# Kernel optimization log

Measured on AMD Instinct MI355X. Metric: run time of the kernel, lower is better.

The kernel has to match this reference:

```python
import jax, jax.numpy as jnp
import numpy as np

B, T, C, H = 2, 2048, 1024, 16
D = C // H  # head_dim = 64

def setup_inputs() -> dict:
    key = jax.random.key(0)
    ks = jax.random.split(key, 5)
    x = jax.random.normal(ks[0], (B, T, C), dtype=jnp.float32)
    Wqkv = jax.random.normal(ks[1], (C, 3 * C), dtype=jnp.float32) * 0.02
    bqkv = jnp.zeros((3 * C,), dtype=jnp.float32)
    Wout = jax.random.normal(ks[2], (C, C), dtype=jnp.float32) * 0.02
    bout = jnp.zeros((C,), dtype=jnp.float32)
    return {"x": x, "Wqkv": Wqkv, "bqkv": bqkv, "Wout": Wout, "bout": bout}

def reference(x, Wqkv, bqkv, Wout, bout):
    Bb, Tt, Cc = x.shape
    qkv = x @ Wqkv + bqkv                       # [B,T,3C]
    qkv = qkv.reshape(Bb, Tt, 3, H, D)
    qkv = jnp.transpose(qkv, (2, 0, 3, 1, 4))   # [3,B,H,T,D]
    q, k, v = qkv[0], qkv[1], qkv[2]
    scale = 1.0 / np.sqrt(D).astype(np.float32)
    scores = jnp.einsum('bhqd,bhkd->bhqk', q, k) * scale  # [B,H,T,T]
    causal = jnp.tril(jnp.ones((Tt, Tt), dtype=bool))
    scores = jnp.where(causal[None, None, :, :], scores, jnp.float32(-jnp.inf))
    attn = jax.nn.softmax(scores, axis=-1)
    out = jnp.einsum('bhqk,bhkd->bhqd', attn, v)          # [B,H,T,D]
    out = jnp.transpose(out, (0, 2, 1, 3)).reshape(Bb, Tt, Cc)
    return out @ Wout + bout
```

## Files before the change

### kernel.cpp

```cpp
#include <hip/hip_runtime.h>

#define Bc 2
#define Tc 2048
#define Cc 1024
#define Hc 16
#define Dc 64
#define Mtot (Bc*Tc)
#define Kdim Cc
#define N1 (3*Cc)
#define N2 Cc

typedef __attribute__((ext_vector_type(8))) short short8;
typedef __attribute__((ext_vector_type(4))) float float4v;
typedef __attribute__((ext_vector_type(2))) unsigned int uint2v;
typedef __attribute__((ext_vector_type(4))) unsigned int uint4v;

#define HAVE_PLSWAP (__has_builtin(__builtin_amdgcn_permlane32_swap) && __has_builtin(__builtin_amdgcn_permlane16_swap))

__device__ __forceinline__ unsigned short f2bf(float f) {
  unsigned int u = __builtin_bit_cast(unsigned int, f);
  u += 0x7FFFu + ((u >> 16) & 1u);
  return (unsigned short)(u >> 16);
}

__device__ __forceinline__ unsigned int pk_bf16(float a, float b) {
#if __has_builtin(__builtin_amdgcn_cvt_pk_bf16_f32)
  typedef __attribute__((ext_vector_type(2))) __bf16 bf16x2;
  bf16x2 v = __builtin_amdgcn_cvt_pk_bf16_f32(a, b);
  return __builtin_bit_cast(unsigned int, v);
#else
  return (unsigned int)f2bf(a) | ((unsigned int)f2bf(b) << 16);
#endif
}

__device__ __forceinline__ float fast_exp2(float x) {
#if __has_builtin(__builtin_amdgcn_exp2f)
  return __builtin_amdgcn_exp2f(x);
#else
  return exp2f(x);
#endif
}

__device__ __forceinline__ void gl2lds16(const unsigned short* g, unsigned short* l) {
  __builtin_amdgcn_global_load_lds((const __attribute__((address_space(1))) void*)g,
                                   (__attribute__((address_space(3))) void*)l, 16, 0, 0);
}

#if HAVE_PLSWAP
__device__ __forceinline__ short8 pv_frag(unsigned int a, unsigned int b,
                                          unsigned int c, unsigned int d) {
  uint2v r0 = __builtin_amdgcn_permlane32_swap(a, c, false, false);
  uint2v r1 = __builtin_amdgcn_permlane16_swap(r0[0], r0[1], false, false);
  uint2v r2 = __builtin_amdgcn_permlane32_swap(b, d, false, false);
  uint2v r3 = __builtin_amdgcn_permlane16_swap(r2[0], r2[1], false, false);
  uint4v w = {r1[0], r3[0], r1[1], r3[1]};
  return __builtin_bit_cast(short8, w);
}
#endif

__global__ __launch_bounds__(256) void k_prep(const float* __restrict__ wqkv,
                                              const float* __restrict__ wout,
                                              const float* __restrict__ x,
                                              unsigned short* __restrict__ wqkvT,
                                              unsigned short* __restrict__ woutT,
                                              unsigned short* __restrict__ xb) {
  const int bx = blockIdx.x;
  if (bx >= 128) {
    int idx = ((bx - 128) * 32 + blockIdx.y) * 256 + threadIdx.x;
    float4 v = ((const float4*)x)[idx];
    uint2 o;
    o.x = pk_bf16(v.x, v.y);
    o.y = pk_bf16(v.z, v.w);
    ((uint2*)xb)[idx] = o;
    return;
  }
  __shared__ float tile[32][33];
  const float* w;  unsigned short* wT;  int N, n0;
  if (bx < 96) { w = wqkv; wT = wqkvT; N = N1; n0 = bx * 32; }
  else         { w = wout; wT = woutT; N = N2; n0 = (bx - 96) * 32; }
  const int k0 = blockIdx.y * 32;
  int tx = threadIdx.x & 31, ty = threadIdx.x >> 5;
  for (int i = 0; i < 4; ++i)
    tile[ty + 8*i][tx] = w[(size_t)(k0 + ty + 8*i) * N + n0 + tx];
  __syncthreads();
  for (int i = 0; i < 4; ++i)
    wT[(size_t)(n0 + ty + 8*i) * Kdim + k0 + tx] = f2bf(tile[tx][ty + 8*i]);
}

__global__ __launch_bounds__(256) void k_gemm_qkv(const unsigned short* __restrict__ A,
                                                  const unsigned short* __restrict__ BT,
                                                  const float* __restrict__ bias,
                                                  unsigned short* __restrict__ qkv) {
  __shared__ alignas(16) unsigned short smem[16384];
  const int m0 = blockIdx.y * 128, n0 = blockIdx.x * 128;
  const int tid = threadIdx.x;
  const int w = tid >> 6, lane = tid & 63;
  const int ln = lane & 15, qd = lane >> 4;
  const int wm = w >> 1, wn = w & 1;
  const int c0 = tid, c1 = tid + 256;
  const int row0 = c0 >> 2, ko0 = (c0 & 3) * 8;
  const int row1 = c1 >> 2, ko1 = (c1 & 3) * 8;
  const float4v zero4 = {0.f, 0.f, 0.f, 0.f};
  float4v acc[4][4];
  for (int i = 0; i < 4; ++i) for (int j = 0; j < 4; ++j) acc[i][j] = zero4;

  gl2lds16(A  + (size_t)(m0 + row0) * Kdim + ko0, smem + c0 * 8);
  gl2lds16(A  + (size_t)(m0 + row1) * Kdim + ko1, smem + c1 * 8);
  gl2lds16(BT + (size_t)(n0 + row0) * Kdim + ko0, smem + 4096 + c0 * 8);
  gl2lds16(BT + (size_t)(n0 + row1) * Kdim + ko1, smem + 4096 + c1 * 8);

  int cur = 0;
  for (int kk = 0; kk < Kdim; kk += 32) {
    __syncthreads();
    if (kk + 32 < Kdim) {
      unsigned short* nb = smem + (cur ^ 1) * 8192;
      gl2lds16(A  + (size_t)(m0 + row0) * Kdim + kk + 32 + ko0, nb + c0 * 8);
      gl2lds16(A  + (size_t)(m0 + row1) * Kdim + kk + 32 + ko1, nb + c1 * 8);
      gl2lds16(BT + (size_t)(n0 + row0) * Kdim + kk + 32 + ko0, nb + 4096 + c0 * 8);
      gl2lds16(BT + (size_t)(n0 + row1) * Kdim + kk + 32 + ko1, nb + 4096 + c1 * 8);
    }
    const unsigned short* As = smem + cur * 8192;
    const unsigned short* Bs = As + 4096;
    short8 af[4], bf[4];
    for (int i = 0; i < 4; ++i)
      af[i] = *(const short8*)(As + (wm*64 + i*16 + ln) * 32 + qd*8);
    for (int j = 0; j < 4; ++j)
      bf[j] = *(const short8*)(Bs + (wn*64 + j*16 + ln) * 32 + qd*8);
    for (int i = 0; i < 4; ++i)
      for (int j = 0; j < 4; ++j)
        acc[i][j] = __builtin_amdgcn_mfma_f32_16x16x32_bf16(af[i], bf[j], acc[i][j], 0, 0, 0);
    cur ^= 1;
  }
  const int s = n0 >> 10;
  if (s < 2) {
    const float scale = (s == 0) ? 0.125f : 1.0f;
    for (int i = 0; i < 4; ++i) {
      int mbase = m0 + wm*64 + i*16 + qd*4;
      for (int j = 0; j < 4; ++j) {
        int ncol = n0 + wn*64 + j*16 + ln;
        float bv = bias[ncol];
        int rem = ncol & 1023;
        int h = rem >> 6, d = rem & 63;
        for (int r = 0; r < 4; ++r) {
          int m = mbase + r;
          int b = m >> 11, t = m & 2047;
          float val = (acc[i][j][r] + bv) * scale;
          qkv[((((size_t)s*Bc + b)*Hc + h)*Tc + t)*Dc + d] = f2bf(val);
        }
      }
    }
  } else {
    unsigned short* vbase = qkv + (size_t)2*Bc*Hc*Tc*Dc;
    const int b = m0 >> 11, t0 = m0 & 2047;
    const int h0 = (n0 & 1023) >> 6;
    for (int p = 0; p < 2; ++p) {
      __syncthreads();
      if (wn == p) {
        for (int i = 0; i < 4; ++i) {
          int tl = wm*64 + i*16 + qd*4;
          for (int j = 0; j < 4; ++j) {
            int dl = j*16 + ln;
            float bv = bias[n0 + p*64 + dl];
            uint2 pk;
            pk.x = pk_bf16(acc[i][j][0] + bv, acc[i][j][1] + bv);
            pk.y = pk_bf16(acc[i][j][2] + bv, acc[i][j][3] + bv);
            *(uint2*)(smem + dl*136 + tl) = pk;
          }
        }
      }
      __syncthreads();
      for (int ii = 0; ii < 4; ++ii) {
        int idx = tid + 256*ii;
        int row = idx >> 4, c16 = idx & 15;
        int4 v = *(const int4*)(smem + row*136 + c16*8);
        *(int4*)(vbase + (((size_t)b*Hc + h0 + p)*Dc + row)*Tc + t0 + c16*8) = v;
      }
    }
  }
}

__global__ __launch_bounds__(256) void k_gemm_out(const unsigned short* __restrict__ A,
                                                  const unsigned short* __restrict__ BT,
                                                  const float* __restrict__ bias,
                                                  float* __restrict__ out) {
  __shared__ alignas(16) unsigned short smem[16384];
  const int m0 = blockIdx.y * 128, n0 = blockIdx.x * 128;
  const int tid = threadIdx.x;
  const int w = tid >> 6, lane = tid & 63;
  const int ln = lane & 15, qd = lane >> 4;
  const int wm = w >> 1, wn = w & 1;
  const int c0 = tid, c1 = tid + 256;
  const int row0 = c0 >> 2, ko0 = (c0 & 3) * 8;
  const int row1 = c1 >> 2, ko1 = (c1 & 3) * 8;
  const float4v zero4 = {0.f, 0.f, 0.f, 0.f};
  float4v acc[4][4];
  for (int i = 0; i < 4; ++i) for (int j = 0; j < 4; ++j) acc[i][j] = zero4;

  gl2lds16(A  + (size_t)(m0 + row0) * Kdim + ko0, smem + c0 * 8);
  gl2lds16(A  + (size_t)(m0 + row1) * Kdim + ko1, smem + c1 * 8);
  gl2lds16(BT + (size_t)(n0 + row0) * Kdim + ko0, smem + 4096 + c0 * 8);
  gl2lds16(BT + (size_t)(n0 + row1) * Kdim + ko1, smem + 4096 + c1 * 8);

  int cur = 0;
  for (int kk = 0; kk < Kdim; kk += 32) {
    __syncthreads();
    if (kk + 32 < Kdim) {
      unsigned short* nb = smem + (cur ^ 1) * 8192;
      gl2lds16(A  + (size_t)(m0 + row0) * Kdim + kk + 32 + ko0, nb + c0 * 8);
      gl2lds16(A  + (size_t)(m0 + row1) * Kdim + kk + 32 + ko1, nb + c1 * 8);
      gl2lds16(BT + (size_t)(n0 + row0) * Kdim + kk + 32 + ko0, nb + 4096 + c0 * 8);
      gl2lds16(BT + (size_t)(n0 + row1) * Kdim + kk + 32 + ko1, nb + 4096 + c1 * 8);
    }
    const unsigned short* As = smem + cur * 8192;
    const unsigned short* Bs = As + 4096;
    short8 af[4], bf[4];
    for (int i = 0; i < 4; ++i)
      af[i] = *(const short8*)(As + (wm*64 + i*16 + ln) * 32 + qd*8);
    for (int j = 0; j < 4; ++j)
      bf[j] = *(const short8*)(Bs + (wn*64 + j*16 + ln) * 32 + qd*8);
    for (int i = 0; i < 4; ++i)
      for (int j = 0; j < 4; ++j)
        acc[i][j] = __builtin_amdgcn_mfma_f32_16x16x32_bf16(af[i], bf[j], acc[i][j], 0, 0, 0);
    cur ^= 1;
  }
  for (int i = 0; i < 4; ++i) {
    int mbase = m0 + wm*64 + i*16 + qd*4;
    for (int j = 0; j < 4; ++j) {
      int ncol = n0 + wn*64 + j*16 + ln;
      float bv = bias[ncol];
      for (int r = 0; r < 4; ++r)
        out[(size_t)(mbase + r) * N2 + ncol] = acc[i][j][r] + bv;
    }
  }
}

__device__ __forceinline__ void attn_substep(
    const short8* kf, const short8* va,
    unsigned short* __restrict__ pw,
    const short8 qa0, const short8 qa1,
    float4v* o, float& l_part,
    int k0, int myq, bool mask, int ln, int qd)
{
  const float L2E = 1.44269504f;
  const float SH = 23.0831098f;
  const float4v zero4 = {0.f, 0.f, 0.f, 0.f};
  float4v s[4];
  for (int ki = 0; ki < 4; ++ki) {
    float4v z = zero4;
    z = __builtin_amdgcn_mfma_f32_16x16x32_bf16(kf[2*ki],     qa0, z, 0, 0, 0);
    s[ki] = __builtin_amdgcn_mfma_f32_16x16x32_bf16(kf[2*ki+1], qa1, z, 0, 0, 0);
  }
  if (mask) {
    for (int ki = 0; ki < 4; ++ki) {
      int key = k0 + ki*16 + qd*4;
      for (int r = 0; r < 4; ++r)
        if (key + r > myq) s[ki][r] = -1e30f;
    }
  }
  float st = 0.f;
  unsigned int pkw[4][2];
  for (int ki = 0; ki < 4; ++ki) {
    float p0 = fast_exp2(fmaf(s[ki][0], L2E, -SH));
    float p1 = fast_exp2(fmaf(s[ki][1], L2E, -SH));
    float p2 = fast_exp2(fmaf(s[ki][2], L2E, -SH));
    float p3 = fast_exp2(fmaf(s[ki][3], L2E, -SH));
    st += (p0 + p1) + (p2 + p3);
    pkw[ki][0] = pk_bf16(p0, p1);
    pkw[ki][1] = pk_bf16(p2, p3);
  }
  l_part += st;
#if HAVE_PLSWAP
  short8 pb0 = pv_frag(pkw[0][0], pkw[0][1], pkw[1][0], pkw[1][1]);
  short8 pb1 = pv_frag(pkw[2][0], pkw[2][1], pkw[3][0], pkw[3][1]);
#else
  for (int ki = 0; ki < 4; ++ki) {
    uint2 pk2; pk2.x = pkw[ki][0]; pk2.y = pkw[ki][1];
    *(uint2*)(pw + ln*72 + ki*16 + qd*4) = pk2;
  }
  short8 pb0 = *(const short8*)(pw + ln*72 + qd*8);
  short8 pb1 = *(const short8*)(pw + ln*72 + 32 + qd*8);
#endif
  for (int dt = 0; dt < 4; ++dt) {
    o[dt] = __builtin_amdgcn_mfma_f32_16x16x32_bf16(va[2*dt],   pb0, o[dt], 0, 0, 0);
    o[dt] = __builtin_amdgcn_mfma_f32_16x16x32_bf16(va[2*dt+1], pb1, o[dt], 0, 0, 0);
  }
}

__global__ __launch_bounds__(256) void k_attn(const unsigned short* __restrict__ qb,
                                              const unsigned short* __restrict__ kb,
                                              const unsigned short* __restrict__ vT,
                                              unsigned short* __restrict__ ob) {
  __shared__ alignas(16) unsigned short Ks[2][64*72];
  __shared__ alignas(16) unsigned short Vt[2][64*72];
#if !HAVE_PLSWAP
  __shared__ alignas(16) unsigned short Ps[4][16*72];
#endif
  const int bh = blockIdx.x;
  const int qt = 31 - blockIdx.y;
  const int tid = threadIdx.x;
  const int w = tid >> 6, lane = tid & 63;
  const int ln = lane & 15, qd = lane >> 4;
  const size_t base = (size_t)bh * Tc * Dc;
  const int b = bh >> 4, h = bh & 15;
  const int srow = tid >> 3, scol = (tid & 7) * 8;
  const float4v zero4 = {0.f, 0.f, 0.f, 0.f};
#if HAVE_PLSWAP
  unsigned short* pw = nullptr;
#else
  unsigned short* pw = Ps[w];
#endif

  const int myq = qt*64 + w*16 + ln;
  const unsigned short* qr = qb + base + (size_t)myq * Dc;
  short8 qa0 = *(const short8*)(qr + qd*8);
  short8 qa1 = *(const short8*)(qr + 32 + qd*8);
  float4v o[4];
  for (int dt = 0; dt < 4; ++dt) o[dt] = zero4;
  float l = 0.f;

  {
    int4 k0v = *(const int4*)(kb + base + (size_t)srow * Dc + scol);
    int4 k1v = *(const int4*)(kb + base + (size_t)(srow + 32) * Dc + scol);
    int4 v0v = *(const int4*)(vT + base + (size_t)srow * Tc + scol);
    int4 v1v = *(const int4*)(vT + base + (size_t)(srow + 32) * Tc + scol);
    *(int4*)(Ks[0] + srow*72 + scol)      = k0v;
    *(int4*)(Ks[0] + (srow+32)*72 + scol) = k1v;
    *(int4*)(Vt[0] + srow*72 + scol)      = v0v;
    *(int4*)(Vt[0] + (srow+32)*72 + scol) = v1v;
  }
  __syncthreads();

  for (int kt = 0; kt <= qt; ++kt) {
    const int cur = kt & 1;
    int4 rk0, rk1, rv0, rv1;
    if (kt < qt) {
      const int k0n = (kt + 1) * 64;
      rk0 = *(const int4*)(kb + base + (size_t)(k0n + srow) * Dc + scol);
      rk1 = *(const int4*)(kb + base + (size_t)(k0n + srow + 32) * Dc + scol);
      rv0 = *(const int4*)(vT + base + (size_t)srow * Tc + k0n + scol);
      rv1 = *(const int4*)(vT + base + (size_t)(srow + 32) * Tc + k0n + scol);
    }
    short8 kf[8], va[8];
    for (int ki = 0; ki < 4; ++ki) {
      const unsigned short* kr = Ks[cur] + (ki*16 + ln)*72;
      kf[2*ki]   = *(const short8*)(kr + qd*8);
      kf[2*ki+1] = *(const short8*)(kr + 32 + qd*8);
    }
    for (int dt = 0; dt < 4; ++dt) {
      const unsigned short* vr = Vt[cur] + (dt*16 + ln)*72;
      va[2*dt]   = *(const short8*)(vr + qd*8);
      va[2*dt+1] = *(const short8*)(vr + 32 + qd*8);
    }
    __builtin_amdgcn_s_setprio(1);
    attn_substep(kf, va, pw, qa0, qa1, o, l, kt*64, myq, kt == qt, ln, qd);
    __builtin_amdgcn_s_setprio(0);
    if (kt < qt) {
      const int nxt = cur ^ 1;
      *(int4*)(Ks[nxt] + srow*72 + scol)      = rk0;
      *(int4*)(Ks[nxt] + (srow+32)*72 + scol) = rk1;
      *(int4*)(Vt[nxt] + srow*72 + scol)      = rv0;
      *(int4*)(Vt[nxt] + (srow+32)*72 + scol) = rv1;
      __syncthreads();
    }
  }
  l += __shfl_xor(l, 16); l += __shfl_xor(l, 32);
  float inv = 1.0f / l;
  for (int dt = 0; dt < 4; ++dt) {
    uint2 ov;
    ov.x = pk_bf16(o[dt][0] * inv, o[dt][1] * inv);
    ov.y = pk_bf16(o[dt][2] * inv, o[dt][3] * inv);
    *(uint2*)(ob + (size_t)(b*Tc + myq)*Cc + h*Dc + dt*16 + qd*4) = ov;
  }
}

extern "C" void kernel_launch(void* const* d_in, const int* in_sizes, int n_in,
                              void* d_out, int out_size, void* d_ws, size_t ws_size,
                              hipStream_t stream) {
  const float* x    = (const float*)d_in[0];
  const float* Wqkv = (const float*)d_in[1];
  const float* bqkv = (const float*)d_in[2];
  const float* Wout = (const float*)d_in[3];
  const float* bout = (const float*)d_in[4];
  float* out = (float*)d_out;

  char* ws = (char*)d_ws;
  unsigned short* xb    = (unsigned short*)ws;
  unsigned short* wqkvT = (unsigned short*)(ws + 8388608);
  unsigned short* woutT = (unsigned short*)(ws + 14680064);
  unsigned short* qkvb  = (unsigned short*)(ws + 16777216);

  k_prep<<<dim3(256, 32), 256, 0, stream>>>(Wqkv, Wout, x, wqkvT, woutT, xb);
  k_gemm_qkv<<<dim3(N1/128, Mtot/128), 256, 0, stream>>>(xb, wqkvT, bqkv, qkvb);
  k_attn<<<dim3(32, 32), 256, 0, stream>>>(qkvb, qkvb + (size_t)Bc*Hc*Tc*Dc,
                                           qkvb + (size_t)2*Bc*Hc*Tc*Dc, xb);
  k_gemm_out<<<dim3(N2/128, Mtot/128), 256, 0, stream>>>(xb, woutT, bout, out);
}
```

Measured before the change: 177.0 us.

## Split attention key tile across warps and swizzle GEMM block order

The attention kernel now assigns each warp two 16-row query fragments and half of the 64-key tile, rather than one query fragment over all keys. K and V fragments loaded from LDS are reused across the two query fragments, and the two key-half partial outputs are combined through shared memory at the end. Both GEMM kernels also remap block indices with a swizzle so that consecutively scheduled blocks share tiles in cache. The costs are more accumulator registers per warp and an extra LDS reduction with two barriers.

```diff
diff --git a/kernel.cpp b/kernel.cpp
--- a/kernel.cpp
+++ b/kernel.cpp
@@ -92,7 +92,9 @@
                                                   const float* __restrict__ bias,
                                                   unsigned short* __restrict__ qkv) {
   __shared__ alignas(16) unsigned short smem[16384];
-  const int m0 = blockIdx.y * 128, n0 = blockIdx.x * 128;
+  const int lin = blockIdx.y * 24 + blockIdx.x;
+  const int swz = (lin & 7) * 96 + (lin >> 3);
+  const int m0 = (swz / 24) * 128, n0 = (swz % 24) * 128;
   const int tid = threadIdx.x;
   const int w = tid >> 6, lane = tid & 63;
   const int ln = lane & 15, qd = lane >> 4;
@@ -184,7 +186,9 @@
                                                   const float* __restrict__ bias,
                                                   float* __restrict__ out) {
   __shared__ alignas(16) unsigned short smem[16384];
-  const int m0 = blockIdx.y * 128, n0 = blockIdx.x * 128;
+  const int lin = blockIdx.y * 8 + blockIdx.x;
+  const int swz = (lin & 7) * 32 + (lin >> 3);
+  const int m0 = (swz >> 3) * 128, n0 = (swz & 7) * 128;
   const int tid = threadIdx.x;
   const int w = tid >> 6, lane = tid & 63;
   const int ln = lane & 15, qd = lane >> 4;
@@ -234,32 +238,32 @@
   }
 }
 
-__device__ __forceinline__ void attn_substep(
+__device__ __forceinline__ void attn_half(
     const short8* kf, const short8* va,
     unsigned short* __restrict__ pw,
     const short8 qa0, const short8 qa1,
     float4v* o, float& l_part,
-    int k0, int myq, bool mask, int ln, int qd)
+    int keybase, int myq, bool mask, int ln, int qd)
 {
   const float L2E = 1.44269504f;
   const float SH = 23.0831098f;
   const float4v zero4 = {0.f, 0.f, 0.f, 0.f};
-  float4v s[4];
-  for (int ki = 0; ki < 4; ++ki) {
+  float4v s[2];
+  for (int ki = 0; ki < 2; ++ki) {
     float4v z = zero4;
     z = __builtin_amdgcn_mfma_f32_16x16x32_bf16(kf[2*ki],     qa0, z, 0, 0, 0);
     s[ki] = __builtin_amdgcn_mfma_f32_16x16x32_bf16(kf[2*ki+1], qa1, z, 0, 0, 0);
   }
   if (mask) {
-    for (int ki = 0; ki < 4; ++ki) {
-      int key = k0 + ki*16 + qd*4;
+    for (int ki = 0; ki < 2; ++ki) {
+      int key = keybase + ki*16 + qd*4;
       for (int r = 0; r < 4; ++r)
         if (key + r > myq) s[ki][r] = -1e30f;
     }
   }
   float st = 0.f;
-  unsigned int pkw[4][2];
-  for (int ki = 0; ki < 4; ++ki) {
+  unsigned int pkw[2][2];
+  for (int ki = 0; ki < 2; ++ki) {
     float p0 = fast_exp2(fmaf(s[ki][0], L2E, -SH));
     float p1 = fast_exp2(fmaf(s[ki][1], L2E, -SH));
     float p2 = fast_exp2(fmaf(s[ki][2], L2E, -SH));
@@ -270,20 +274,16 @@
   }
   l_part += st;
 #if HAVE_PLSWAP
-  short8 pb0 = pv_frag(pkw[0][0], pkw[0][1], pkw[1][0], pkw[1][1]);
-  short8 pb1 = pv_frag(pkw[2][0], pkw[2][1], pkw[3][0], pkw[3][1]);
+  short8 pb = pv_frag(pkw[0][0], pkw[0][1], pkw[1][0], pkw[1][1]);
 #else
-  for (int ki = 0; ki < 4; ++ki) {
+  for (int ki = 0; ki < 2; ++ki) {
     uint2 pk2; pk2.x = pkw[ki][0]; pk2.y = pkw[ki][1];
     *(uint2*)(pw + ln*72 + ki*16 + qd*4) = pk2;
   }
-  short8 pb0 = *(const short8*)(pw + ln*72 + qd*8);
-  short8 pb1 = *(const short8*)(pw + ln*72 + 32 + qd*8);
-#endif
-  for (int dt = 0; dt < 4; ++dt) {
-    o[dt] = __builtin_amdgcn_mfma_f32_16x16x32_bf16(va[2*dt],   pb0, o[dt], 0, 0, 0);
-    o[dt] = __builtin_amdgcn_mfma_f32_16x16x32_bf16(va[2*dt+1], pb1, o[dt], 0, 0, 0);
-  }
+  short8 pb = *(const short8*)(pw + ln*72 + qd*8);
+#endif
+  for (int dt = 0; dt < 4; ++dt)
+    o[dt] = __builtin_amdgcn_mfma_f32_16x16x32_bf16(va[dt], pb, o[dt], 0, 0, 0);
 }
 
 __global__ __launch_bounds__(256) void k_attn(const unsigned short* __restrict__ qb,
@@ -300,6 +300,7 @@
   const int tid = threadIdx.x;
   const int w = tid >> 6, lane = tid & 63;
   const int ln = lane & 15, qd = lane >> 4;
+  const int kw = w >> 1, qw = w & 1;
   const size_t base = (size_t)bh * Tc * Dc;
   const int b = bh >> 4, h = bh & 15;
   const int srow = tid >> 3, scol = (tid & 7) * 8;
@@ -310,13 +311,16 @@
   unsigned short* pw = Ps[w];
 #endif
 
-  const int myq = qt*64 + w*16 + ln;
-  const unsigned short* qr = qb + base + (size_t)myq * Dc;
-  short8 qa0 = *(const short8*)(qr + qd*8);
-  short8 qa1 = *(const short8*)(qr + 32 + qd*8);
-  float4v o[4];
-  for (int dt = 0; dt < 4; ++dt) o[dt] = zero4;
-  float l = 0.f;
+  int myq[2]; short8 qa[2][2];
+  for (int f = 0; f < 2; ++f) {
+    myq[f] = qt*64 + (qw*2 + f)*16 + ln;
+    const unsigned short* qr = qb + base + (size_t)myq[f] * Dc;
+    qa[f][0] = *(const short8*)(qr + qd*8);
+    qa[f][1] = *(const short8*)(qr + 32 + qd*8);
+  }
+  float4v o[2][4];
+  for (int f = 0; f < 2; ++f) for (int dt = 0; dt < 4; ++dt) o[f][dt] = zero4;
+  float l[2] = {0.f, 0.f};
 
   {
     int4 k0v = *(const int4*)(kb + base + (size_t)srow * Dc + scol);
@@ -340,19 +344,19 @@
       rv0 = *(const int4*)(vT + base + (size_t)srow * Tc + k0n + scol);
       rv1 = *(const int4*)(vT + base + (size_t)(srow + 32) * Tc + k0n + scol);
     }
-    short8 kf[8], va[8];
-    for (int ki = 0; ki < 4; ++ki) {
-      const unsigned short* kr = Ks[cur] + (ki*16 + ln)*72;
+    short8 kf[4], va[4];
+    for (int ki = 0; ki < 2; ++ki) {
+      const unsigned short* kr = Ks[cur] + (kw*32 + ki*16 + ln)*72;
       kf[2*ki]   = *(const short8*)(kr + qd*8);
       kf[2*ki+1] = *(const short8*)(kr + 32 + qd*8);
     }
-    for (int dt = 0; dt < 4; ++dt) {
-      const unsigned short* vr = Vt[cur] + (dt*16 + ln)*72;
-      va[2*dt]   = *(const short8*)(vr + qd*8);
-      va[2*dt+1] = *(const short8*)(vr + 32 + qd*8);
-    }
+    for (int dt = 0; dt < 4; ++dt)
+      va[dt] = *(const short8*)(Vt[cur] + (dt*16 + ln)*72 + kw*32 + qd*8);
+    const int keybase = kt*64 + kw*32;
+    const bool mask = (kt == qt);
     __builtin_amdgcn_s_setprio(1);
-    attn_substep(kf, va, pw, qa0, qa1, o, l, kt*64, myq, kt == qt, ln, qd);
+    attn_half(kf, va, pw, qa[0][0], qa[0][1], o[0], l[0], keybase, myq[0], mask, ln, qd);
+    attn_half(kf, va, pw, qa[1][0], qa[1][1], o[1], l[1], keybase, myq[1], mask, ln, qd);
     __builtin_amdgcn_s_setprio(0);
     if (kt < qt) {
       const int nxt = cur ^ 1;
@@ -363,13 +367,37 @@
       __syncthreads();
     }
   }
-  l += __shfl_xor(l, 16); l += __shfl_xor(l, 32);
-  float inv = 1.0f / l;
-  for (int dt = 0; dt < 4; ++dt) {
-    uint2 ov;
-    ov.x = pk_bf16(o[dt][0] * inv, o[dt][1] * inv);
-    ov.y = pk_bf16(o[dt][2] * inv, o[dt][3] * inv);
-    *(uint2*)(ob + (size_t)(b*Tc + myq)*Cc + h*Dc + dt*16 + qd*4) = ov;
+  for (int f = 0; f < 2; ++f) {
+    l[f] += __shfl_xor(l[f], 16);
+    l[f] += __shfl_xor(l[f], 32);
+  }
+  float* red = (float*)Ks;
+  __syncthreads();
+  if (kw) {
+    float* slot = red + (qw*64 + lane)*34;
+    for (int f = 0; f < 2; ++f)
+      for (int dt = 0; dt < 4; ++dt)
+        for (int r = 0; r < 4; ++r)
+          slot[f*16 + dt*4 + r] = o[f][dt][r];
+    slot[32] = l[0]; slot[33] = l[1];
+  }
+  __syncthreads();
+  if (!kw) {
+    const float* slot = red + (qw*64 + lane)*34;
+    for (int f = 0; f < 2; ++f)
+      for (int dt = 0; dt < 4; ++dt)
+        for (int r = 0; r < 4; ++r)
+          o[f][dt][r] += slot[f*16 + dt*4 + r];
+    l[0] += slot[32]; l[1] += slot[33];
+    for (int f = 0; f < 2; ++f) {
+      float inv = 1.0f / l[f];
+      for (int dt = 0; dt < 4; ++dt) {
+        uint2 ov;
+        ov.x = pk_bf16(o[f][dt][0] * inv, o[f][dt][1] * inv);
+        ov.y = pk_bf16(o[f][dt][2] * inv, o[f][dt][3] * inv);
+        *(uint2*)(ob + (size_t)(b*Tc + myq[f])*Cc + h*Dc + dt*16 + qd*4) = ov;
+      }
+    }
   }
 }
 
```

Measured after the change: 179.8 us. No clear change (+1.6%).
